# Optimization experiments

Hardware: AMD Instinct MI355X
Metric: run time of the kernel (lower is better)

The kernel has to match this reference:

```python
import jax, jax.numpy as jnp
import numpy as np
from jax import lax

B, N = 4, 192
D_IN = 768       # bert hidden
H = 512          # lstm_hid_size (bidirectional)
HD = H // 2
DIST_E = 20
TYPE_E = 20
CONV_IN = H + DIST_E + TYPE_E   # 552
CONV_H = 96
DILATIONS = (1, 2, 3)
BIAFF = 512
CLS = 10
N_POS = 30
SIZE_E = 25


def setup_inputs() -> dict:
    key = jax.random.key(0)
    ks = iter(jax.random.split(key, 48))

    def nrm(shape, s):
        return jax.random.normal(next(ks), shape, jnp.float32) * s

    word_reps = jax.random.normal(next(ks), (B, N, D_IN), jnp.float32)
    word_length = jnp.concatenate([
        jnp.array([N], jnp.int32),
        jax.random.randint(next(ks), (B - 1,), N // 2, N + 1).astype(jnp.int32)])
    dist_inputs = jax.random.randint(next(ks), (B, N, N), 0, 20)
    ar = jnp.arange(N)
    valid = (ar[None, :, None] < word_length[:, None, None]) & (ar[None, None, :] < word_length[:, None, None])
    loss_mask = valid.astype(jnp.int32)
    return dict(
        word_reps=word_reps, word_length=word_length, dist_inputs=dist_inputs, loss_mask=loss_mask,
        lstm_Wih_f=nrm((4 * HD, D_IN), 0.03), lstm_Whh_f=nrm((4 * HD, HD), 0.03), lstm_b_f=jnp.zeros((4 * HD,), jnp.float32),
        lstm_Wih_b=nrm((4 * HD, D_IN), 0.03), lstm_Whh_b=nrm((4 * HD, HD), 0.03), lstm_b_b=jnp.zeros((4 * HD,), jnp.float32),
        cln_gamma=jnp.ones((H,), jnp.float32), cln_beta=jnp.zeros((H,), jnp.float32),
        cln_Wg=nrm((H, H), 0.02), cln_Wb=nrm((H, H), 0.02),
        dis_emb=nrm((20, DIST_E), 0.1), reg_emb=nrm((3, TYPE_E), 0.1),
        conv_base_w=nrm((1, 1, CONV_IN, CONV_H), 0.05), conv_base_b=jnp.zeros((CONV_H,), jnp.float32),
        conv_dw_w=nrm((len(DILATIONS), 3, 3, 1, CONV_H), 0.05), conv_dw_b=jnp.zeros((len(DILATIONS), CONV_H), jnp.float32),
        mlp1_w=nrm((BIAFF, H), 0.04), mlp1_b=jnp.zeros((BIAFF,), jnp.float32),
        mlp2_w=nrm((BIAFF, H), 0.04), mlp2_b=jnp.zeros((BIAFF,), jnp.float32),
        head_w=nrm((BIAFF, H), 0.04), head_b=jnp.zeros((BIAFF,), jnp.float32),
        tail_w=nrm((BIAFF, H), 0.04), tail_b=jnp.zeros((BIAFF,), jnp.float32),
        biaff_W=nrm((CLS, BIAFF + 1, BIAFF + 1), 0.02),
        size_emb=nrm((N_POS, SIZE_E), 0.1),
        W_co=nrm((CLS, 2 * (BIAFF + 1) + SIZE_E), 0.02),
    )


def _lstm_dir(x, mask, Wih, Whh, b):
    # x: [B,T,D], mask: [B,T] bool. PyTorch LSTM (packed): padded steps emit 0, state frozen.
    xw = jnp.einsum('btd,gd->btg', x, Wih) + b  # precomputed input projection, gate order i,f,g,o
    h0 = jnp.zeros((x.shape[0], Whh.shape[1]), x.dtype)

    def step(carry, inp):
        h, c = carry
        xw_t, m_t = inp
        gates = xw_t + h @ Whh.T
        i, f, g, o = jnp.split(gates, 4, axis=-1)
        c_new = jax.nn.sigmoid(f) * c + jax.nn.sigmoid(i) * jnp.tanh(g)
        h_new = jax.nn.sigmoid(o) * jnp.tanh(c_new)
        m = m_t[:, None]
        h = jnp.where(m, h_new, h)
        c = jnp.where(m, c_new, c)
        return (h, c), jnp.where(m, h_new, 0.0)

    _, hs = lax.scan(step, (h0, h0), (xw.transpose(1, 0, 2), mask.T))
    return hs.transpose(1, 0, 2)


def _conv2d_nhwc(x, w, b, dil, groups):
    pad = (w.shape[0] - 1) // 2 * dil
    y = lax.conv_general_dilated(
        x, w, window_strides=(1, 1), padding=[(pad, pad), (pad, pad)],
        rhs_dilation=(dil, dil),
        dimension_numbers=('NHWC', 'HWIO', 'NHWC'),
        feature_group_count=groups)
    return y + b


def _forward(word_reps, lstm_Wih_f, lstm_Whh_f, lstm_b_f, lstm_Wih_b, lstm_Whh_b, lstm_b_b,
             cln_gamma, cln_beta, cln_Wg, cln_Wb, dis_emb, reg_emb,
             conv_base_w, conv_base_b, conv_dw_w, conv_dw_b,
             mlp1_w, mlp1_b, mlp2_w, mlp2_b, head_w, head_b, tail_w, tail_b,
             biaff_W, size_emb, W_co,
             word_length, dist_inputs, loss_mask):
    Bsz, T, _ = word_reps.shape
    ar = jnp.arange(T)
    seq_mask = ar[None, :] < word_length[:, None]

    # --- BiLSTM over packed (length-masked) sequences ---
    fwd = _lstm_dir(word_reps, seq_mask, lstm_Wih_f, lstm_Whh_f, lstm_b_f)
    idx = jnp.clip(word_length[:, None] - 1 - ar[None, :], 0, T - 1)  # reverse within each length
    x_rev = jnp.take_along_axis(word_reps, idx[:, :, None], axis=1)
    bwd_rev = _lstm_dir(x_rev, seq_mask, lstm_Wih_b, lstm_Whh_b, lstm_b_b)
    bwd = jnp.take_along_axis(bwd_rev, idx[:, :, None], axis=1) * seq_mask[:, :, None]
    wr = jnp.concatenate([fwd, bwd], axis=-1)  # [B,T,H]

    # --- conditional LayerNorm: normalize wr[i], scale/shift conditioned on wr[j] ---
    mu = wr.mean(-1, keepdims=True)
    xc = wr - mu
    var = (xc * xc).mean(-1, keepdims=True)
    ln = xc / jnp.sqrt(var + 1e-12)                 # [B,T,H]
    w_cond = cln_gamma + wr @ cln_Wg.T              # [B,T,H]
    b_cond = cln_beta + wr @ cln_Wb.T
    cln = ln[:, :, None, :] * w_cond[:, None, :, :] + b_cond[:, None, :, :]  # [B,T,T,H]

    dis = dis_emb[dist_inputs]                      # [B,T,T,20]
    reg_inputs = jnp.tril(loss_mask) + loss_mask    # values in {0,1,2}
    reg = reg_emb[reg_inputs]                       # [B,T,T,20]
    grid_mask = (loss_mask != 0)[..., None]
    conv_in = jnp.where(grid_mask, jnp.concatenate([dis, reg, cln], axis=-1), 0.0)

    # --- dilated depthwise conv stack (act='leakyrelu') ---
    x = jax.nn.leaky_relu(_conv2d_nhwc(conv_in, conv_base_w, conv_base_b, 1, 1))
    outs = []
    for i, d in enumerate(DILATIONS):
        x = jax.nn.leaky_relu(_conv2d_nhwc(x, conv_dw_w[i], conv_dw_b[i], d, CONV_H))
        outs.append(x)
    conv_out = jnp.where(grid_mask, jnp.concatenate(outs, axis=-1), 0.0)
    del conv_out  # computed in source, but CoPredictor.forward ignores z (faithful)

    # --- CoPredictor ---
    gelu = lambda v: jax.nn.gelu(v, approximate=False)
    h = gelu(wr @ mlp1_w.T + mlp1_b)
    t = gelu(wr @ mlp2_w.T + mlp2_b)
    ones = jnp.ones(h.shape[:-1] + (1,), h.dtype)
    h1 = jnp.concatenate([h, ones], -1)
    t1 = jnp.concatenate([t, ones], -1)
    o1 = jnp.einsum('bxi,oij,byj->bxyo', h1, biaff_W, t1)  # [B,T,T,CLS]

    head = jnp.concatenate([jax.nn.leaky_relu(wr @ head_w.T + head_b), ones], -1)  # [B,T,P]
    tail = jnp.concatenate([jax.nn.leaky_relu(wr @ tail_w.T + tail_b), ones], -1)
    span = ar[None, :] - ar[:, None]
    span = jnp.clip(span, -(N_POS // 2), N_POS // 2 - 1) + N_POS // 2
    se = size_emb[span]  # [T,T,SIZE_E]
    P = BIAFF + 1
    # einsum over the concat [head|tail|size] split into three partial products (no [B,T,T,1051] materialization)
    o3 = (jnp.einsum('bmi,ki->bkm', head, W_co[:, :P])[:, :, :, None]
          + jnp.einsum('bni,ki->bkn', tail, W_co[:, P:2 * P])[:, :, None, :]
          + jnp.einsum('mns,ks->kmn', se, W_co[:, 2 * P:])[None])
    return jnp.transpose(o1, (0, 3, 1, 2)) + o3  # [B,CLS,T,T]


def reference(word_reps, word_length, dist_inputs, loss_mask,
              lstm_Wih_f, lstm_Whh_f, lstm_b_f, lstm_Wih_b, lstm_Whh_b, lstm_b_b,
              cln_gamma, cln_beta, cln_Wg, cln_Wb, dis_emb, reg_emb,
              conv_base_w, conv_base_b, conv_dw_w, conv_dw_b,
              mlp1_w, mlp1_b, mlp2_w, mlp2_b, head_w, head_b, tail_w, tail_b,
              biaff_W, size_emb, W_co):
    return _forward(word_reps, lstm_Wih_f, lstm_Whh_f, lstm_b_f, lstm_Wih_b, lstm_Whh_b, lstm_b_b,
                    cln_gamma, cln_beta, cln_Wg, cln_Wb, dis_emb, reg_emb,
                    conv_base_w, conv_base_b, conv_dw_w, conv_dw_b,
                    mlp1_w, mlp1_b, mlp2_w, mlp2_b, head_w, head_b, tail_w, tail_b,
                    biaff_W, size_emb, W_co,
                    word_length, dist_inputs, loss_mask)
```

## Files before the change

### kernel.cpp

```cpp
#include <hip/hip_runtime.h>
#include <math.h>

#define BB 4
#define NN 192
#define DIN 768
#define HD 256
#define HH 512
#define PP 513
#define CLS 10
#define NBIG 5130
#define KP 544
#define WCO_LD 1051
#define LMAX 192

typedef __attribute__((ext_vector_type(8))) __bf16 bf16x8;
typedef __attribute__((ext_vector_type(4))) float f32x4;
typedef unsigned short u16;
typedef unsigned int u32;
typedef unsigned long long u64;

__device__ __forceinline__ float sigf(float x) { return 1.f / (1.f + expf(-x)); }

__device__ __forceinline__ u16 f2bf(float f) {
    u32 x = __float_as_uint(f);
    u32 r = (x + 0x7FFF + ((x >> 16) & 1)) >> 16;
    return (u16)r;
}
__device__ __forceinline__ float bf2f(u16 h) {
    return __uint_as_float(((u32)h) << 16);
}

__global__ void mega_prep(const float* __restrict__ word_reps,
                          const float* __restrict__ Wih_f, const float* __restrict__ Wih_b,
                          const float* __restrict__ b_f, const float* __restrict__ b_b,
                          const float* __restrict__ mlp1_w, const float* __restrict__ mlp2_w,
                          const float* __restrict__ head_w, const float* __restrict__ tail_w,
                          const float* __restrict__ mlp1_b, const float* __restrict__ mlp2_b,
                          const float* __restrict__ head_b, const float* __restrict__ tail_b,
                          const float* __restrict__ Whh_f, const float* __restrict__ Whh_b,
                          u16* __restrict__ wrph, u16* __restrict__ wrpl,
                          u16* __restrict__ wihh, u16* __restrict__ wihl, float* __restrict__ bias_ih,
                          u16* __restrict__ mwh, u16* __restrict__ mwl, float* __restrict__ bias_mid,
                          u16* __restrict__ pw)
{
    int i = blockIdx.x * blockDim.x + threadIdx.x;
    if (i < 589824) {
        float v = word_reps[i];
        u16 h = f2bf(v);
        wrph[i] = h; wrpl[i] = f2bf(v - bf2f(h));
        return;
    }
    i -= 589824;
    if (i < 1572864) {
        int n = i / 768, k = i - n * 768;
        float v = (n < 1024) ? Wih_f[(size_t)n * 768 + k] : Wih_b[(size_t)(n - 1024) * 768 + k];
        u16 h = f2bf(v);
        wihh[i] = h; wihl[i] = f2bf(v - bf2f(h));
        return;
    }
    i -= 1572864;
    if (i < 1048576) {
        int n = i >> 9, k = i & 511;
        const float* Ws = (n < 512) ? mlp1_w : (n < 1024) ? mlp2_w : (n < 1536) ? head_w : tail_w;
        float v = Ws[(size_t)(n & 511) * 512 + k];
        u16 h = f2bf(v);
        mwh[i] = h; mwl[i] = f2bf(v - bf2f(h));
        return;
    }
    i -= 1048576;
    if (i < 524288) {
        int f = i;
        int e = f & 7;
        int lane = (f >> 3) & 63;
        int frag = (f >> 9) & 31;
        int wave = (f >> 14) & 7;
        int dh = f >> 17;
        int dir = dh >> 1, half = dh & 1;
        int kt = frag >> 2, t = frag & 3;
        int col = half * 512 + wave * 64 + t * 16 + (lane & 15);
        int u = col >> 2, gt = col & 3;
        int g = gt * 256 + u;
        int k = kt * 32 + (lane >> 4) * 8 + e;
        const float* W = dir ? Whh_b : Whh_f;
        pw[f] = f2bf(W[(size_t)g * 256 + k]);
        return;
    }
    i -= 524288;
    if (i < 2048) {
        bias_ih[i] = (i < 1024) ? b_f[i] : b_b[i - 1024];
        return;
    }
    i -= 2048;
    if (i < 2048) {
        bias_mid[i] = (i < 512) ? mlp1_b[i] : (i < 1024) ? mlp2_b[i - 512]
                    : (i < 1536) ? head_b[i - 1024] : tail_b[i - 1536];
    }
}

__global__ void wsplit_kernel(const float* __restrict__ W, u16* __restrict__ Wh,
                              u16* __restrict__ Wl)
{
    __shared__ float tile[32][33];
    int kc = blockIdx.z, k0 = blockIdx.x * 32, j0 = blockIdx.y * 32;
    int tx = threadIdx.x, ty = threadIdx.y;
#pragma unroll
    for (int yy = 0; yy < 32; yy += 8) {
        int k = k0 + ty + yy, j = j0 + tx;
        tile[ty + yy][tx] = (k < 513 && j < 513) ? W[((size_t)kc * 513 + k) * 513 + j] : 0.f;
    }
    __syncthreads();
#pragma unroll
    for (int yy = 0; yy < 32; yy += 8) {
        int j = j0 + ty + yy, k = k0 + tx;
        if (j < 513 && k < KP) {
            float v = tile[tx][ty + yy];
            size_t o = ((size_t)kc * 513 + j) * KP + k;
            u16 h = f2bf(v);
            Wh[o] = h; Wl[o] = f2bf(v - bf2f(h));
        }
    }
}

__global__ __launch_bounds__(256)
void gemm_mfma_hl(const u16* __restrict__ Ah, const u16* __restrict__ Al,
                  const u16* __restrict__ Bh, const u16* __restrict__ Bl,
                  const float* __restrict__ bias, float* __restrict__ C,
                  int K, int ldc, int act)
{
    const int lane = threadIdx.x & 63, w = threadIdx.x >> 6;
    const int m0 = blockIdx.y * 64;
    const int n0 = blockIdx.x * 64 + w * 16;
    const int arow = m0 + (lane & 15);
    const int brow = n0 + (lane & 15);
    const int koff = (lane >> 4) * 8;
    f32x4 acc[4] = {};

    for (int k0 = 0; k0 < K; k0 += 32) {
        bf16x8 bh = *(const bf16x8*)(Bh + (size_t)brow * K + k0 + koff);
        bf16x8 bl = *(const bf16x8*)(Bl + (size_t)brow * K + k0 + koff);
#pragma unroll
        for (int mi = 0; mi < 4; ++mi) {
            size_t ao = (size_t)(arow + mi * 16) * K + k0 + koff;
            bf16x8 ah = *(const bf16x8*)(Ah + ao);
            bf16x8 al = *(const bf16x8*)(Al + ao);
            acc[mi] = __builtin_amdgcn_mfma_f32_16x16x32_bf16(ah, bh, acc[mi], 0, 0, 0);
            acc[mi] = __builtin_amdgcn_mfma_f32_16x16x32_bf16(ah, bl, acc[mi], 0, 0, 0);
            acc[mi] = __builtin_amdgcn_mfma_f32_16x16x32_bf16(al, bh, acc[mi], 0, 0, 0);
        }
    }
    const int cn = n0 + (lane & 15);
    const float bv = bias ? bias[cn] : 0.f;
    const int am = (act == 3) ? (cn < 1024 ? 1 : 2) : act;
#pragma unroll
    for (int mi = 0; mi < 4; ++mi)
#pragma unroll
        for (int r = 0; r < 4; ++r) {
            int m = m0 + mi * 16 + (lane >> 4) * 4 + r;
            float v = acc[mi][r] + bv;
            if (am == 1) v = 0.5f * v * (1.f + erff(v * 0.70710678118654752f));
            else if (am == 2) v = v > 0.f ? v : 0.01f * v;
            C[(size_t)m * ldc + cn] = v;
        }
}

__global__ __launch_bounds__(256)
void biaff_mfma(const u16* __restrict__ Ah, const u16* __restrict__ Al,
                const u16* __restrict__ Wh, const u16* __restrict__ Wl,
                u16* __restrict__ Mh, u16* __restrict__ Ml)
{
    const int lane = threadIdx.x & 63, w = threadIdx.x >> 6;
    const int m0 = blockIdx.y * 64;
    const int n0 = blockIdx.x * 128 + w * 32;
    const int arow = m0 + (lane & 15);
    const int koff = (lane >> 4) * 8;
    f32x4 acc[4][2] = {};

    for (int c = 0; c < 17; ++c) {
        const int k0 = c * 32 + koff;
        bf16x8 bh[2], bl[2];
#pragma unroll
        for (int ni = 0; ni < 2; ++ni) {
            size_t bo = (size_t)(n0 + ni * 16 + (lane & 15)) * KP + k0;
            bh[ni] = *(const bf16x8*)(Wh + bo);
            bl[ni] = *(const bf16x8*)(Wl + bo);
        }
#pragma unroll
        for (int mi = 0; mi < 4; ++mi) {
            size_t ao = (size_t)(arow + mi * 16) * KP + k0;
            bf16x8 ah = *(const bf16x8*)(Ah + ao);
            bf16x8 al = *(const bf16x8*)(Al + ao);
#pragma unroll
            for (int ni = 0; ni < 2; ++ni) {
                acc[mi][ni] = __builtin_amdgcn_mfma_f32_16x16x32_bf16(ah, bh[ni], acc[mi][ni], 0, 0, 0);
                acc[mi][ni] = __builtin_amdgcn_mfma_f32_16x16x32_bf16(ah, bl[ni], acc[mi][ni], 0, 0, 0);
                acc[mi][ni] = __builtin_amdgcn_mfma_f32_16x16x32_bf16(al, bh[ni], acc[mi][ni], 0, 0, 0);
            }
        }
    }
#pragma unroll
    for (int mi = 0; mi < 4; ++mi)
#pragma unroll
        for (int ni = 0; ni < 2; ++ni) {
            int n = n0 + ni * 16 + (lane & 15);
            if (n < NBIG) {
                int kc = n / PP, j = n - kc * PP;
#pragma unroll
                for (int r = 0; r < 4; ++r) {
                    int m = m0 + mi * 16 + (lane >> 4) * 4 + r;
                    float v = acc[mi][ni][r];
                    u16 h = f2bf(v);
                    size_t o = (size_t)m * (CLS * KP) + kc * KP + j;
                    Mh[o] = h; Ml[o] = f2bf(v - bf2f(h));
                }
            }
        }
}

__global__ __launch_bounds__(256)
void final_mfma(const u16* __restrict__ Mh, const u16* __restrict__ Ml,
                const u16* __restrict__ Th, const u16* __restrict__ Tl,
                const float* __restrict__ hv, const float* __restrict__ tv,
                const float* __restrict__ Tt, float* __restrict__ out)
{
    const int lane = threadIdx.x & 63, w = threadIdx.x >> 6;
    const int r0 = blockIdx.y * 64;
    const int b = r0 / 1920;
    const int rem = r0 - b * 1920;
    const int kc = rem / 192;
    const int x0 = rem - kc * 192;
    const int n0 = blockIdx.x * 64 + w * 16;
    const int koff = (lane >> 4) * 8;
    const size_t abase = (size_t)(b * 192 + x0 + (lane & 15)) * (CLS * KP) + kc * KP;
    const size_t bbase = (size_t)(b * 192 + n0 + (lane & 15)) * KP;
    f32x4 acc[4] = {};

    for (int c = 0; c < 17; ++c) {
        const int k0 = c * 32 + koff;
        bf16x8 bh = *(const bf16x8*)(Th + bbase + k0);
        bf16x8 bl = *(const bf16x8*)(Tl + bbase + k0);
#pragma unroll
        for (int mi = 0; mi < 4; ++mi) {
            size_t ao = abase + (size_t)mi * 16 * (CLS * KP) + k0;
            bf16x8 ah = *(const bf16x8*)(Mh + ao);
            bf16x8 al = *(const bf16x8*)(Ml + ao);
            acc[mi] = __builtin_amdgcn_mfma_f32_16x16x32_bf16(ah, bh, acc[mi], 0, 0, 0);
            acc[mi] = __builtin_amdgcn_mfma_f32_16x16x32_bf16(ah, bl, acc[mi], 0, 0, 0);
            acc[mi] = __builtin_amdgcn_mfma_f32_16x16x32_bf16(al, bh, acc[mi], 0, 0, 0);
        }
    }
    const int bk = b * 10 + kc;
    const int y = n0 + (lane & 15);
    const float tvv = tv[bk * 192 + y];
#pragma unroll
    for (int mi = 0; mi < 4; ++mi)
#pragma unroll
        for (int r = 0; r < 4; ++r) {
            int x = x0 + mi * 16 + (lane >> 4) * 4 + r;
            int d = y - x;
            d = d < -15 ? -15 : (d > 14 ? 14 : d);
            float v = acc[mi][r] + hv[bk * 192 + x] + tvv + Tt[kc * 30 + d + 15];
            out[(size_t)(bk * 192 + x) * 192 + y] = v;
        }
}

__global__ __launch_bounds__(512, 1)
void lstm_mfma(const float* __restrict__ xw, const u16* __restrict__ pw,
               const int* __restrict__ wl,
               u16* __restrict__ wrsh, u16* __restrict__ wrsl,
               u64* __restrict__ ex)
{
    const int dh = blockIdx.x;
    const int dir = dh >> 1, half = dh & 1;
    const int tid = threadIdx.x;
    const int lane = tid & 63, wid = tid >> 6;

    __shared__ __align__(16) u16 h_hi[16 * 256];
    __shared__ __align__(16) u16 h_lo[16 * 256];
    __shared__ __align__(16) float gates_s[512 * 4];

    for (int i = tid; i < 16 * 256; i += 512) { h_hi[i] = 0; h_lo[i] = 0; }

    bf16x8 bw[32];
    {
        const u16* base = pw + ((size_t)(dh * 8 + wid) * 32 * 64 + lane) * 8;
#pragma unroll
        for (int i = 0; i < 32; ++i)
            bw[i] = *reinterpret_cast<const bf16x8*>(base + (size_t)i * 64 * 8);
    }

    const int u_loc = tid >> 2, bb = tid & 3;
    const int u_glob = half * 128 + u_loc;
    const int Lb = wl[bb];
    float c_state = 0.f, h_state = 0.f;

    const int row = lane & 15, quad = lane >> 4;
    const int abase = row * 512 + quad * 16;
    const int aswz = (row & 7) << 4;
    const int wswz = bb << 4;

    __syncthreads();

    f32x4 acc[4];
    for (int t = 0; t < LMAX; ++t) {
        int ttok = (dir == 0) ? t : (Lb - 1 - t);
        if (ttok < 0) ttok = 0;
        const float* xrow = xw + ((size_t)(bb * 192 + ttok)) * 2048 + dir * 1024 + u_glob;
        float x0 = xrow[0], x1 = xrow[256], x2 = xrow[512], x3 = xrow[768];

#pragma unroll
        for (int tt = 0; tt < 4; ++tt) acc[tt] = (f32x4){0.f, 0.f, 0.f, 0.f};
#pragma unroll
        for (int kt = 0; kt < 8; ++kt) {
            int off = (abase + kt * 64) ^ aswz;
            bf16x8 ah = *reinterpret_cast<const bf16x8*>((const char*)h_hi + off);
            bf16x8 al = *reinterpret_cast<const bf16x8*>((const char*)h_lo + off);
#pragma unroll
            for (int tt = 0; tt < 4; ++tt) {
                acc[tt] = __builtin_amdgcn_mfma_f32_16x16x32_bf16(ah, bw[kt * 4 + tt], acc[tt], 0, 0, 0);
                acc[tt] = __builtin_amdgcn_mfma_f32_16x16x32_bf16(al, bw[kt * 4 + tt], acc[tt], 0, 0, 0);
            }
        }
        if (lane < 16) {
#pragma unroll
            for (int tt = 0; tt < 4; ++tt) {
                int col_loc = wid * 64 + tt * 16 + lane;
                *reinterpret_cast<f32x4*>(&gates_s[col_loc * 4]) = acc[tt];
            }
        }
        __syncthreads();

        float gi = gates_s[(u_loc * 4 + 0) * 4 + bb] + x0;
        float gf = gates_s[(u_loc * 4 + 1) * 4 + bb] + x1;
        float gg = gates_s[(u_loc * 4 + 2) * 4 + bb] + x2;
        float go = gates_s[(u_loc * 4 + 3) * 4 + bb] + x3;
        float cn = sigf(gf) * c_state + sigf(gi) * tanhf(gg);
        float hn = sigf(go) * tanhf(cn);
        if (t < Lb) { c_state = cn; h_state = hn; }
        u16 hi_b = f2bf(h_state);
        u16 lo_b = f2bf(h_state - bf2f(hi_b));
        if (t < Lb) {
            size_t wo = ((size_t)(bb * 192 + ttok)) * 512 + dir * 256 + u_glob;
            wrsh[wo] = hi_b; wrsl[wo] = lo_b;
        }
        {
            int lb = (bb * 512 + u_glob * 2) ^ wswz;
            *(u16*)((char*)h_hi + lb) = hi_b;
            *(u16*)((char*)h_lo + lb) = lo_b;
        }
        u32 packv = ((u32)lo_b << 16) | hi_b;

        u64 vv = (u64)packv | ((u64)(u32)(t + 1) << 32);
        __hip_atomic_store(&ex[((size_t)dh * 2 + (t & 1)) * 512 + tid], vv,
                           __ATOMIC_RELAXED, __HIP_MEMORY_SCOPE_AGENT);
        u64 pv;
        do {
            pv = __hip_atomic_load(&ex[((size_t)(dh ^ 1) * 2 + (t & 1)) * 512 + tid],
                                   __ATOMIC_RELAXED, __HIP_MEMORY_SCOPE_AGENT);
            if ((u32)(pv >> 32) == (u32)(t + 1)) break;
            __builtin_amdgcn_s_sleep(1);
        } while (true);
        {
            u32 pk = (u32)pv;
            int pu = (half ^ 1) * 128 + (tid >> 2);
            int lb = (bb * 512 + pu * 2) ^ wswz;
            *(u16*)((char*)h_hi + lb) = (u16)(pk & 0xFFFFu);
            *(u16*)((char*)h_lo + lb) = (u16)(pk >> 16);
        }
        __syncthreads();
    }
}

__global__ void split_ht(const float* __restrict__ HT, u16* __restrict__ h1h,
                         u16* __restrict__ h1l, u16* __restrict__ t1h,
                         u16* __restrict__ t1l)
{
    int idx = blockIdx.x * blockDim.x + threadIdx.x;
    if (idx >= 768 * KP) return;
    int m = idx / KP, k = idx - m * KP;
    float hv = (k < 512) ? HT[(size_t)m * 2048 + k] : (k == 512 ? 1.f : 0.f);
    float tv = (k < 512) ? HT[(size_t)m * 2048 + 512 + k] : (k == 512 ? 1.f : 0.f);
    u16 hh = f2bf(hv);
    h1h[idx] = hh; h1l[idx] = f2bf(hv - bf2f(hh));
    u16 th = f2bf(tv);
    t1h[idx] = th; t1l[idx] = f2bf(tv - bf2f(th));
}

__global__ __launch_bounds__(256)
void hvtv_ttab(const float* __restrict__ HT, const float* __restrict__ Wco,
               const float* __restrict__ size_emb,
               float* __restrict__ hv, float* __restrict__ tv, float* __restrict__ Tt)
{
    int bk = blockIdx.x;
    if (bk < 40) {
        int b = bk / 10, k = bk - (bk / 10) * 10;
        int wave = threadIdx.x >> 6, lane = threadIdx.x & 63;
        const float* wk = Wco + k * WCO_LD;
        for (int x = wave; x < 192; x += 4) {
            const float* hrow = HT + (size_t)(b * 192 + x) * 2048 + 1024;
            float sh = 0.f, st = 0.f;
            for (int i = lane; i < 512; i += 64) {
                sh = fmaf(hrow[i], wk[i], sh);
                st = fmaf(hrow[512 + i], wk[513 + i], st);
            }
#pragma unroll
            for (int o = 32; o; o >>= 1) {
                sh += __shfl_down(sh, o);
                st += __shfl_down(st, o);
            }
            if (lane == 0) {
                hv[bk * 192 + x] = sh + wk[512];
                tv[bk * 192 + x] = st + wk[1025];
            }
        }
    } else {
        int idx = (bk - 40) * 256 + threadIdx.x;
        if (idx < 300) {
            int k = idx / 30, p = idx - (idx / 30) * 30;
            float s = 0.f;
            for (int e = 0; e < 25; ++e)
                s = fmaf(size_emb[p * 25 + e], Wco[k * WCO_LD + 1026 + e], s);
            Tt[idx] = s;
        }
    }
}

extern "C" void kernel_launch(void* const* d_in, const int* in_sizes, int n_in,
                              void* d_out, int out_size, void* d_ws, size_t ws_size,
                              hipStream_t stream)
{
    const float* word_reps = (const float*)d_in[0];
    const int*   word_length = (const int*)d_in[1];
    const float* Wih_f = (const float*)d_in[4];
    const float* Whh_f = (const float*)d_in[5];
    const float* b_f   = (const float*)d_in[6];
    const float* Wih_b = (const float*)d_in[7];
    const float* Whh_b = (const float*)d_in[8];
    const float* b_b   = (const float*)d_in[9];
    const float* mlp1_w = (const float*)d_in[20];
    const float* mlp1_b = (const float*)d_in[21];
    const float* mlp2_w = (const float*)d_in[22];
    const float* mlp2_b = (const float*)d_in[23];
    const float* head_w = (const float*)d_in[24];
    const float* head_b = (const float*)d_in[25];
    const float* tail_w = (const float*)d_in[26];
    const float* tail_b = (const float*)d_in[27];
    const float* biaffW = (const float*)d_in[28];
    const float* size_emb = (const float*)d_in[29];
    const float* W_co = (const float*)d_in[30];

    float* W = (float*)d_ws;
    float* xw   = W;
    u16*  wrsh  = (u16*)(W + 1572864);
    u16*  wrsl  = (u16*)(W + 1769472);
    u16*  pw    = (u16*)(W + 1966080);
    u16*  Mbh   = (u16*)W;
    float* HT   = W + 2228224;
    u16* h1h = (u16*)(W + 3801088);
    u16* h1l = (u16*)(W + 4009984);
    u16* t1h = (u16*)(W + 4218880);
    u16* t1l = (u16*)(W + 4427776);
    u16* Wsph = (u16*)(W + 4636672);
    u16* Wspl = (u16*)(W + 6064128);
    u16* Mbl  = (u16*)(W + 7491584);
    u16* wihh = (u16*)(W + 7491584);
    u16* wihl = (u16*)(W + 8278016);
    float* bias_ih = W + 9064448;
    float* hv = W + 9580544;
    float* tv = W + 9588224;
    float* Tt = W + 9595904;
    u64* ex   = (u64*)(W + 9596208);
    u16* wrph = (u16*)(W + 9604400);
    u16* wrpl = (u16*)(W + 9899312);
    u16* mwh  = (u16*)(W + 10194224);
    u16* mwl  = (u16*)(W + 10718512);
    float* bias_mid = W + 11242800;

    hipMemsetAsync(wrsh, 0, (size_t)393216 * 2 * sizeof(u16), stream);
    hipMemsetAsync(ex, 0, (size_t)4096 * 8, stream);

    mega_prep<<<(3739648 + 255) / 256, 256, 0, stream>>>(
        word_reps, Wih_f, Wih_b, b_f, b_b,
        mlp1_w, mlp2_w, head_w, tail_w, mlp1_b, mlp2_b, head_b, tail_b,
        Whh_f, Whh_b,
        wrph, wrpl, wihh, wihl, bias_ih, mwh, mwl, bias_mid, pw);

    wsplit_kernel<<<dim3(17, 17, 10), dim3(32, 8), 0, stream>>>(biaffW, Wsph, Wspl);

    gemm_mfma_hl<<<dim3(32, 12), 256, 0, stream>>>(wrph, wrpl, wihh, wihl, bias_ih, xw, 768, 2048, 0);

    lstm_mfma<<<4, 512, 0, stream>>>(xw, pw, word_length, wrsh, wrsl, ex);

    gemm_mfma_hl<<<dim3(32, 12), 256, 0, stream>>>(wrsh, wrsl, mwh, mwl, bias_mid, HT, 512, 2048, 3);

    split_ht<<<(768 * KP + 255) / 256, 256, 0, stream>>>(HT, h1h, h1l, t1h, t1l);
    hvtv_ttab<<<42, 256, 0, stream>>>(HT, W_co, size_emb, hv, tv, Tt);

    hipMemsetAsync(Mbh, 0, (size_t)4177920 * 2, stream);
    hipMemsetAsync(Mbl, 0, (size_t)4177920 * 2, stream);

    biaff_mfma<<<dim3(41, 12), 256, 0, stream>>>(h1h, h1l, Wsph, Wspl, Mbh, Mbl);
    final_mfma<<<dim3(3, 120), 256, 0, stream>>>(Mbh, Mbl, t1h, t1l, hv, tv, Tt, (float*)d_out);
}
```

Before: 860.4 us.

## Overlap LSTM exchange with half-K MFMA, fuse prep kernels and drop memsets

Each LSTM block now computes the half of the recurrent matmul that uses its own hidden units first, then waits for the partner block's half of h. This hides the cross-block spin-wait behind MFMA work. The biaffine weight split is moved into extra blocks of the LSTM launch so it runs alongside the serial recurrence. split_ht and hvtv_ttab are merged into one launch, and the full memsets of the biaffine intermediate are replaced by zeroing only the pad columns inside biaff_mfma. This saves launches and memory traffic but adds complexity, and extra blocks could contend with the 4 recurrent blocks.

```diff
diff --git a/kernel.cpp b/kernel.cpp
--- a/kernel.cpp
+++ b/kernel.cpp
@@ -97,30 +97,6 @@
     }
 }
 
-__global__ void wsplit_kernel(const float* __restrict__ W, u16* __restrict__ Wh,
-                              u16* __restrict__ Wl)
-{
-    __shared__ float tile[32][33];
-    int kc = blockIdx.z, k0 = blockIdx.x * 32, j0 = blockIdx.y * 32;
-    int tx = threadIdx.x, ty = threadIdx.y;
-#pragma unroll
-    for (int yy = 0; yy < 32; yy += 8) {
-        int k = k0 + ty + yy, j = j0 + tx;
-        tile[ty + yy][tx] = (k < 513 && j < 513) ? W[((size_t)kc * 513 + k) * 513 + j] : 0.f;
-    }
-    __syncthreads();
-#pragma unroll
-    for (int yy = 0; yy < 32; yy += 8) {
-        int j = j0 + ty + yy, k = k0 + tx;
-        if (j < 513 && k < KP) {
-            float v = tile[tx][ty + yy];
-            size_t o = ((size_t)kc * 513 + j) * KP + k;
-            u16 h = f2bf(v);
-            Wh[o] = h; Wl[o] = f2bf(v - bf2f(h));
-        }
-    }
-}
-
 __global__ __launch_bounds__(256)
 void gemm_mfma_hl(const u16* __restrict__ Ah, const u16* __restrict__ Al,
                   const u16* __restrict__ Bh, const u16* __restrict__ Bl,
@@ -168,6 +144,15 @@
                 const u16* __restrict__ Wh, const u16* __restrict__ Wl,
                 u16* __restrict__ Mh, u16* __restrict__ Ml)
 {
+    {
+        int gtid = (blockIdx.y * 41 + blockIdx.x) * 256 + threadIdx.x;
+        for (int p = gtid; p < 238080; p += 125952) {
+            int m = p / 310, r2 = p - m * 310;
+            int kc = r2 / 31, jj = 513 + (r2 - kc * 31);
+            size_t o = (size_t)m * (CLS * KP) + kc * KP + jj;
+            Mh[o] = 0; Ml[o] = 0;
+        }
+    }
     const int lane = threadIdx.x & 63, w = threadIdx.x >> 6;
     const int m0 = blockIdx.y * 64;
     const int n0 = blockIdx.x * 128 + w * 32;
@@ -267,8 +252,37 @@
 void lstm_mfma(const float* __restrict__ xw, const u16* __restrict__ pw,
                const int* __restrict__ wl,
                u16* __restrict__ wrsh, u16* __restrict__ wrsl,
-               u64* __restrict__ ex)
-{
+               u64* __restrict__ ex,
+               const float* __restrict__ biaffW,
+               u16* __restrict__ Wsph, u16* __restrict__ Wspl)
+{
+    if (blockIdx.x >= 4) {
+        __shared__ float tile2[2][32][33];
+        const int sub = threadIdx.x >> 8;
+        const int tx = threadIdx.x & 31, ty = (threadIdx.x >> 5) & 7;
+        const int tt = (blockIdx.x - 4) * 2 + sub;
+        int kc = tt / 289, rem = tt - kc * 289;
+        int k0 = (rem % 17) * 32, j0 = (rem / 17) * 32;
+#pragma unroll
+        for (int yy = 0; yy < 32; yy += 8) {
+            int k = k0 + ty + yy, j = j0 + tx;
+            tile2[sub][ty + yy][tx] = (k < 513 && j < 513)
+                ? biaffW[((size_t)kc * 513 + k) * 513 + j] : 0.f;
+        }
+        __syncthreads();
+#pragma unroll
+        for (int yy = 0; yy < 32; yy += 8) {
+            int j = j0 + ty + yy, k = k0 + tx;
+            if (j < 513 && k < KP) {
+                float v = tile2[sub][tx][ty + yy];
+                size_t o = ((size_t)kc * 513 + j) * KP + k;
+                u16 h = f2bf(v);
+                Wsph[o] = h; Wspl[o] = f2bf(v - bf2f(h));
+            }
+        }
+        return;
+    }
+
     const int dh = blockIdx.x;
     const int dir = dh >> 1, half = dh & 1;
     const int tid = threadIdx.x;
@@ -297,6 +311,9 @@
     const int abase = row * 512 + quad * 16;
     const int aswz = (row & 7) << 4;
     const int wswz = bb << 4;
+
+    const int kl0 = half * 4;
+    const int kr0 = 4 - half * 4;
 
     __syncthreads();
 
@@ -310,7 +327,37 @@
 #pragma unroll
         for (int tt = 0; tt < 4; ++tt) acc[tt] = (f32x4){0.f, 0.f, 0.f, 0.f};
 #pragma unroll
-        for (int kt = 0; kt < 8; ++kt) {
+        for (int k2 = 0; k2 < 4; ++k2) {
+            const int kt = kl0 + k2;
+            int off = (abase + kt * 64) ^ aswz;
+            bf16x8 ah = *reinterpret_cast<const bf16x8*>((const char*)h_hi + off);
+            bf16x8 al = *reinterpret_cast<const bf16x8*>((const char*)h_lo + off);
+#pragma unroll
+            for (int tt = 0; tt < 4; ++tt) {
+                acc[tt] = __builtin_amdgcn_mfma_f32_16x16x32_bf16(ah, bw[kt * 4 + tt], acc[tt], 0, 0, 0);
+                acc[tt] = __builtin_amdgcn_mfma_f32_16x16x32_bf16(al, bw[kt * 4 + tt], acc[tt], 0, 0, 0);
+            }
+        }
+
+        if (t > 0) {
+            const u64* pp = &ex[((size_t)(dh ^ 1) * 2 + (t & 1)) * 512 + tid];
+            u64 pv;
+            do {
+                pv = __hip_atomic_load(pp, __ATOMIC_RELAXED, __HIP_MEMORY_SCOPE_AGENT);
+                if ((u32)(pv >> 32) == (u32)t) break;
+                __builtin_amdgcn_s_sleep(1);
+            } while (true);
+            u32 pk = (u32)pv;
+            int pu = (half ^ 1) * 128 + u_loc;
+            int lb2 = (bb * 512 + pu * 2) ^ wswz;
+            *(u16*)((char*)h_hi + lb2) = (u16)(pk & 0xFFFFu);
+            *(u16*)((char*)h_lo + lb2) = (u16)(pk >> 16);
+        }
+        __syncthreads();
+
+#pragma unroll
+        for (int k2 = 0; k2 < 4; ++k2) {
+            const int kt = kr0 + k2;
             int off = (abase + kt * 64) ^ aswz;
             bf16x8 ah = *reinterpret_cast<const bf16x8*>((const char*)h_hi + off);
             bf16x8 al = *reinterpret_cast<const bf16x8*>((const char*)h_lo + off);
@@ -338,57 +385,30 @@
         if (t < Lb) { c_state = cn; h_state = hn; }
         u16 hi_b = f2bf(h_state);
         u16 lo_b = f2bf(h_state - bf2f(hi_b));
+
+        u64 vv = (u64)(((u32)lo_b << 16) | hi_b) | ((u64)(u32)(t + 1) << 32);
+        __hip_atomic_store(&ex[((size_t)dh * 2 + ((t + 1) & 1)) * 512 + tid], vv,
+                           __ATOMIC_RELAXED, __HIP_MEMORY_SCOPE_AGENT);
+
         if (t < Lb) {
             size_t wo = ((size_t)(bb * 192 + ttok)) * 512 + dir * 256 + u_glob;
             wrsh[wo] = hi_b; wrsl[wo] = lo_b;
         }
         {
-            int lb = (bb * 512 + u_glob * 2) ^ wswz;
-            *(u16*)((char*)h_hi + lb) = hi_b;
-            *(u16*)((char*)h_lo + lb) = lo_b;
-        }
-        u32 packv = ((u32)lo_b << 16) | hi_b;
-
-        u64 vv = (u64)packv | ((u64)(u32)(t + 1) << 32);
-        __hip_atomic_store(&ex[((size_t)dh * 2 + (t & 1)) * 512 + tid], vv,
-                           __ATOMIC_RELAXED, __HIP_MEMORY_SCOPE_AGENT);
-        u64 pv;
-        do {
-            pv = __hip_atomic_load(&ex[((size_t)(dh ^ 1) * 2 + (t & 1)) * 512 + tid],
-                                   __ATOMIC_RELAXED, __HIP_MEMORY_SCOPE_AGENT);
-            if ((u32)(pv >> 32) == (u32)(t + 1)) break;
-            __builtin_amdgcn_s_sleep(1);
-        } while (true);
-        {
-            u32 pk = (u32)pv;
-            int pu = (half ^ 1) * 128 + (tid >> 2);
-            int lb = (bb * 512 + pu * 2) ^ wswz;
-            *(u16*)((char*)h_hi + lb) = (u16)(pk & 0xFFFFu);
-            *(u16*)((char*)h_lo + lb) = (u16)(pk >> 16);
+            int lb2 = (bb * 512 + u_glob * 2) ^ wswz;
+            *(u16*)((char*)h_hi + lb2) = hi_b;
+            *(u16*)((char*)h_lo + lb2) = lo_b;
         }
         __syncthreads();
     }
 }
 
-__global__ void split_ht(const float* __restrict__ HT, u16* __restrict__ h1h,
-                         u16* __restrict__ h1l, u16* __restrict__ t1h,
-                         u16* __restrict__ t1l)
-{
-    int idx = blockIdx.x * blockDim.x + threadIdx.x;
-    if (idx >= 768 * KP) return;
-    int m = idx / KP, k = idx - m * KP;
-    float hv = (k < 512) ? HT[(size_t)m * 2048 + k] : (k == 512 ? 1.f : 0.f);
-    float tv = (k < 512) ? HT[(size_t)m * 2048 + 512 + k] : (k == 512 ? 1.f : 0.f);
-    u16 hh = f2bf(hv);
-    h1h[idx] = hh; h1l[idx] = f2bf(hv - bf2f(hh));
-    u16 th = f2bf(tv);
-    t1h[idx] = th; t1l[idx] = f2bf(tv - bf2f(th));
-}
-
 __global__ __launch_bounds__(256)
-void hvtv_ttab(const float* __restrict__ HT, const float* __restrict__ Wco,
-               const float* __restrict__ size_emb,
-               float* __restrict__ hv, float* __restrict__ tv, float* __restrict__ Tt)
+void post_ht(const float* __restrict__ HT, const float* __restrict__ Wco,
+             const float* __restrict__ size_emb,
+             u16* __restrict__ h1h, u16* __restrict__ h1l,
+             u16* __restrict__ t1h, u16* __restrict__ t1l,
+             float* __restrict__ hv, float* __restrict__ tv, float* __restrict__ Tt)
 {
     int bk = blockIdx.x;
     if (bk < 40) {
@@ -412,7 +432,7 @@
                 tv[bk * 192 + x] = st + wk[1025];
             }
         }
-    } else {
+    } else if (bk < 42) {
         int idx = (bk - 40) * 256 + threadIdx.x;
         if (idx < 300) {
             int k = idx / 30, p = idx - (idx / 30) * 30;
@@ -420,6 +440,17 @@
             for (int e = 0; e < 25; ++e)
                 s = fmaf(size_emb[p * 25 + e], Wco[k * WCO_LD + 1026 + e], s);
             Tt[idx] = s;
+        }
+    } else {
+        int idx = (bk - 42) * 256 + threadIdx.x;
+        if (idx < 768 * KP) {
+            int m = idx / KP, k = idx - m * KP;
+            float hvv = (k < 512) ? HT[(size_t)m * 2048 + k] : (k == 512 ? 1.f : 0.f);
+            float tvv = (k < 512) ? HT[(size_t)m * 2048 + 512 + k] : (k == 512 ? 1.f : 0.f);
+            u16 hh = f2bf(hvv);
+            h1h[idx] = hh; h1l[idx] = f2bf(hvv - bf2f(hh));
+            u16 th = f2bf(tvv);
+            t1h[idx] = th; t1l[idx] = f2bf(tvv - bf2f(th));
         }
     }
 }
@@ -484,19 +515,15 @@
         Whh_f, Whh_b,
         wrph, wrpl, wihh, wihl, bias_ih, mwh, mwl, bias_mid, pw);
 
-    wsplit_kernel<<<dim3(17, 17, 10), dim3(32, 8), 0, stream>>>(biaffW, Wsph, Wspl);
-
     gemm_mfma_hl<<<dim3(32, 12), 256, 0, stream>>>(wrph, wrpl, wihh, wihl, bias_ih, xw, 768, 2048, 0);
 
-    lstm_mfma<<<4, 512, 0, stream>>>(xw, pw, word_length, wrsh, wrsl, ex);
+    lstm_mfma<<<1449, 512, 0, stream>>>(xw, pw, word_length, wrsh, wrsl, ex,
+                                        biaffW, Wsph, Wspl);
 
     gemm_mfma_hl<<<dim3(32, 12), 256, 0, stream>>>(wrsh, wrsl, mwh, mwl, bias_mid, HT, 512, 2048, 3);
 
-    split_ht<<<(768 * KP + 255) / 256, 256, 0, stream>>>(HT, h1h, h1l, t1h, t1l);
-    hvtv_ttab<<<42, 256, 0, stream>>>(HT, W_co, size_emb, hv, tv, Tt);
-
-    hipMemsetAsync(Mbh, 0, (size_t)4177920 * 2, stream);
-    hipMemsetAsync(Mbl, 0, (size_t)4177920 * 2, stream);
+    post_ht<<<42 + 1632, 256, 0, stream>>>(HT, W_co, size_emb,
+                                           h1h, h1l, t1h, t1l, hv, tv, Tt);
 
     biaff_mfma<<<dim3(41, 12), 256, 0, stream>>>(h1h, h1l, Wsph, Wspl, Mbh, Mbl);
     final_mfma<<<dim3(3, 120), 256, 0, stream>>>(Mbh, Mbl, t1h, t1l, hv, tv, Tt, (float*)d_out);
```

Measured after the change: 1.957 ms. 2.27x slower.
